# Kernel optimization log

Hardware: AMD Instinct MI355X
Metric: run time of the kernel (lower is better)

## Reference

```python
import jax, jax.numpy as jnp
import numpy as np

N, E, D, V, MAX_EDGES, G, ITERS = 50000, 200000, 128, 2000, 3, 256, 2


def _mlp3(h, W1, b1, W2, b2, W3, b3):
    h = jax.nn.relu(h @ W1 + b1)
    h = jax.nn.relu(h @ W2 + b2)
    return jax.nn.relu(h @ W3 + b3)


def _enc(ids, emb, W1, b1, W2, b2):
    h = emb[ids]
    h = jax.nn.relu(h @ W1 + b1)
    return jax.nn.relu(h @ W2 + b2)


def setup_inputs():
    key = jax.random.key(0)
    ks = iter(jax.random.split(key, 64))

    def p(shape):
        return jax.random.normal(next(ks), shape, jnp.float32) * 0.02

    inp = {
        'x': jax.random.randint(next(ks), (N,), 0, V),
        'edge_index': jax.random.randint(next(ks), (2, E), 0, N),
        'edge_attr': jax.random.randint(next(ks), (E,), 0, MAX_EDGES),
        'batch_vec': jnp.sort(jax.random.randint(next(ks), (N,), 0, G)),
        'emb_node': p((V, 2 * D)), 'Wn1': p((2 * D, D)), 'bn1': jnp.zeros((D,), jnp.float32),
        'Wn2': p((D, D)), 'bn2': jnp.zeros((D,), jnp.float32),
        'emb_edge': p((MAX_EDGES, 2 * D)), 'We1': p((2 * D, D)), 'be1': jnp.zeros((D,), jnp.float32),
        'We2': p((D, D)), 'be2': jnp.zeros((D,), jnp.float32),
    }
    for tag in ('p', 'c', 'f'):  # parent_agg, child_agg, final_agg 3-layer MLPs
        inp['W' + tag + '1'] = p((3 * D, 2 * D)); inp['b' + tag + '1'] = jnp.zeros((2 * D,), jnp.float32)
        inp['W' + tag + '2'] = p((2 * D, D)); inp['b' + tag + '2'] = jnp.zeros((D,), jnp.float32)
        inp['W' + tag + '3'] = p((D, D)); inp['b' + tag + '3'] = jnp.zeros((D,), jnp.float32)
    inp['Wo1'] = p((D, 4 * D)); inp['bo1'] = jnp.zeros((4 * D,), jnp.float32)
    inp['Wo2'] = p((4 * D, 8 * D)); inp['bo2'] = jnp.zeros((8 * D,), jnp.float32)
    return inp


def reference(x, edge_index, edge_attr, batch_vec, emb_node, Wn1, bn1, Wn2, bn2,
              emb_edge, We1, be1, We2, be2,
              Wp1, bp1, Wp2, bp2, Wp3, bp3,
              Wc1, bc1, Wc2, bc2, Wc3, bc3,
              Wf1, bf1, Wf2, bf2, Wf3, bf3,
              Wo1, bo1, Wo2, bo2):
    nodes = _enc(x, emb_node, Wn1, bn1, Wn2, bn2)       # [N, D]
    ea = _enc(edge_attr, emb_edge, We1, be1, We2, be2)  # [E, D]
    src, dst = edge_index[0], edge_index[1]
    # both aggregations normalize by degree of edge_index[0] (as in the source)
    deg = jax.ops.segment_sum(jnp.ones((E,), nodes.dtype), src, num_segments=N)
    deg_inv = jnp.where(deg > 0, 1.0 / deg, 0.0)[:, None]  # [N, 1]
    for _ in range(ITERS):
        # parent agg: flow source_to_target -> x_i = nodes[dst], x_j = nodes[src], sum at dst
        mp = _mlp3(jnp.concatenate([nodes[dst], nodes[src], ea], axis=1), Wp1, bp1, Wp2, bp2, Wp3, bp3)
        fi = deg_inv * jax.ops.segment_sum(mp, dst, num_segments=N)
        # child agg: flow target_to_source -> x_i = nodes[src], x_j = nodes[dst], sum at src
        mc = _mlp3(jnp.concatenate([nodes[src], nodes[dst], ea], axis=1), Wc1, bc1, Wc2, bc2, Wc3, bc3)
        fo = deg_inv * jax.ops.segment_sum(mc, src, num_segments=N)
        upd = _mlp3(jnp.concatenate([nodes, fi, fo], axis=1), Wf1, bf1, Wf2, bf2, Wf3, bf3)
        nodes = nodes + upd
    h = jax.nn.relu(nodes @ Wo1 + bo1)
    h = jax.nn.relu(h @ Wo2 + bo2)                      # [N, 8D]
    return jax.ops.segment_max(h, batch_vec, num_segments=G)  # global max pool [G, 8D]
```

## Files before the change

### kernel.cpp

```cpp
#include <hip/hip_runtime.h>

#define NN 50000
#define NE 200000
#define DD 128
#define GG 256
#define NITERS 2
#define NBINS 50176
#define NPART 196

typedef unsigned short u16;
typedef unsigned int u32;
typedef __bf16 bf16x8 __attribute__((ext_vector_type(8)));
typedef float f32x4 __attribute__((ext_vector_type(4)));

union U16x8 { uint4 u; bf16x8 v; u16 s[8]; };

__device__ __forceinline__ u16 f2b(float f) {
    u32 u = __float_as_uint(f);
    return (u16)((u + 0x7FFFu + ((u >> 16) & 1u)) >> 16);
}
__device__ __forceinline__ float b2f(u16 s) { return __uint_as_float(((u32)s) << 16); }

__device__ __forceinline__ uint2 pack4(const float* v) {
    uint2 r;
    r.x = (u32)f2b(v[0]) | ((u32)f2b(v[1]) << 16);
    r.y = (u32)f2b(v[2]) | ((u32)f2b(v[3]) << 16);
    return r;
}

__device__ __forceinline__ void gload_lds16(const void* g, void* lds) {
    __builtin_amdgcn_global_load_lds((const __attribute__((address_space(1))) void*)g,
                                     (__attribute__((address_space(3))) void*)lds, 16, 0, 0);
}

__device__ __forceinline__ int xcd_swz(int orig, int nwg) {
    int q = nwg >> 3, r = nwg & 7;
    int x = orig & 7, loc = orig >> 3;
    return (x < r ? x * (q + 1) : r * (q + 1) + (x - r) * q) + loc;
}

template<int K, int NL, int EPI, bool RELU, int LDN>
__global__ __launch_bounds__(256) void expand_k(
    const u16* __restrict__ A, const uint4* __restrict__ wfrag,
    const float* __restrict__ bias, float* __restrict__ of, u16* __restrict__ ob,
    int M)
{
    constexpr int KS = K / 32;
    __shared__ uint4 smem[K * 16];
    const int t = threadIdx.x, l = t & 63, wv = t >> 6;
    const int mh = wv >> 1, nh = wv & 1;
    const int mblk = blockIdx.x;

    #pragma unroll
    for (int i = 0; i < K / 16; ++i) {
        int s = t + 256 * i;
        int ln = s & 63, mt = (s >> 6) & 7, ksl = s >> 9;
        int row = mblk * 128 + mt * 16 + (ln & 15);
        if (row >= M) row = M - 1;
        int kk = ksl * 32 + (ln >> 4) * 8;
        gload_lds16(A + (size_t)row * K + kk, &smem[s - ln]);
    }
    __syncthreads();

    for (int c = 0; c < NL; ++c) {
        f32x4 acc[4][4] = {};
        #pragma unroll
        for (int ksl = 0; ksl < KS; ++ksl) {
            uint4 wa[4];
            #pragma unroll
            for (int mi = 0; mi < 4; ++mi)
                wa[mi] = wfrag[(size_t)((c * KS + ksl) * 8 + mh * 4 + mi) * 64 + l];
            bf16x8 bn[4];
            #pragma unroll
            for (int ni = 0; ni < 4; ++ni) { U16x8 u; u.u = smem[(ksl * 8 + nh * 4 + ni) * 64 + l]; bn[ni] = u.v; }
            #pragma unroll
            for (int mi = 0; mi < 4; ++mi) {
                U16x8 u; u.u = wa[mi];
                #pragma unroll
                for (int ni = 0; ni < 4; ++ni)
                    acc[mi][ni] = __builtin_amdgcn_mfma_f32_16x16x32_bf16(u.v, bn[ni], acc[mi][ni], 0, 0, 0);
            }
        }
        float4 bb[4];
        #pragma unroll
        for (int mi = 0; mi < 4; ++mi) {
            if (bias) bb[mi] = *(const float4*)(bias + c * 128 + mh * 64 + mi * 16 + 4 * (l >> 4));
            else { bb[mi].x = 0.f; bb[mi].y = 0.f; bb[mi].z = 0.f; bb[mi].w = 0.f; }
        }
        #pragma unroll
        for (int ni = 0; ni < 4; ++ni) {
            int node = mblk * 128 + nh * 64 + ni * 16 + (l & 15);
            if (node >= M) continue;
            #pragma unroll
            for (int mi = 0; mi < 4; ++mi) {
                int col = c * 128 + mh * 64 + mi * 16 + 4 * (l >> 4);
                float v[4];
                const float* bf = &bb[mi].x;
                #pragma unroll
                for (int r = 0; r < 4; ++r) {
                    v[r] = acc[mi][ni][r] + bf[r];
                    if (RELU) v[r] = fmaxf(v[r], 0.f);
                }
                if (EPI == 0) {
                    *(uint2*)(ob + (size_t)node * LDN + col) = pack4(v);
                } else {
                    size_t a = (size_t)node * 128 + col;
                    if (EPI == 2) {
                        float4 old = *(const float4*)(of + a);
                        v[0] += old.x; v[1] += old.y; v[2] += old.z; v[3] += old.w;
                    }
                    float4 s4; s4.x = v[0]; s4.y = v[1]; s4.z = v[2]; s4.w = v[3];
                    *(float4*)(of + a) = s4;
                    *(uint2*)(ob + a) = pack4(v);
                }
            }
        }
    }
}

struct SrcBf16 {
    static constexpr bool DIRECT = true;
    const u16* A; int K;
    __device__ const void* gaddr(int row, int kk) const { return A + (size_t)row * K + kk; }
    __device__ bf16x8 operator()(int row, int kk) const {
        U16x8 u; u.u = *(const uint4*)(A + (size_t)row * K + kk); return u.v;
    }
};
struct SrcEnc {
    static constexpr bool DIRECT = false;
    const float* emb; const int* xids;
    __device__ const void* gaddr(int, int) const { return nullptr; }
    __device__ bf16x8 operator()(int row, int kk) const {
        int n = xids[row];
        const float* p = emb + (size_t)n * 256 + kk;
        float4 f0 = *(const float4*)p, f1 = *(const float4*)(p + 4);
        U16x8 r;
        r.s[0]=f2b(f0.x); r.s[1]=f2b(f0.y); r.s[2]=f2b(f0.z); r.s[3]=f2b(f0.w);
        r.s[4]=f2b(f1.x); r.s[5]=f2b(f1.y); r.s[6]=f2b(f1.z); r.s[7]=f2b(f1.w);
        return r.v;
    }
};
struct SrcUpd {
    static constexpr bool DIRECT = false;
    const float* nodes; const float* fi; const float* fo; const float* deg;
    __device__ const void* gaddr(int, int) const { return nullptr; }
    __device__ bf16x8 operator()(int row, int kk) const {
        const float* s; float sc = 1.f;
        if (kk < 128) s = nodes + (size_t)row * 128 + kk;
        else {
            float d = deg[row];
            sc = d > 0.f ? 1.f / d : 0.f;
            s = (kk < 256) ? fi + (size_t)row * 128 + (kk - 128)
                           : fo + (size_t)row * 128 + (kk - 256);
        }
        float4 f0 = *(const float4*)s, f1 = *(const float4*)(s + 4);
        U16x8 r;
        r.s[0]=f2b(f0.x*sc); r.s[1]=f2b(f0.y*sc); r.s[2]=f2b(f0.z*sc); r.s[3]=f2b(f0.w*sc);
        r.s[4]=f2b(f1.x*sc); r.s[5]=f2b(f1.y*sc); r.s[6]=f2b(f1.z*sc); r.s[7]=f2b(f1.w*sc);
        return r.v;
    }
};

struct EpiArgs { float* of; u16* ob; const int* idx; int ldN; };

template<int KDIM, int NBLK, int EPI, bool RELU, class SRC>
__global__ __launch_bounds__(256) void gemm_k(SRC src, const uint4* __restrict__ wfrag,
                                              const float* __restrict__ bias,
                                              EpiArgs ea, int M)
{
    constexpr int KS = KDIM / 32;
    constexpr int NPANEL = KDIM / 64;
    __shared__ uint4 smem[2048];
    const int t = threadIdx.x;
    const int l = t & 63;
    const int wv = t >> 6;
    const int mh = wv >> 1, nh = wv & 1;
    const int ell = xcd_swz(blockIdx.x, gridDim.x);
    const int mblk = ell / NBLK, nblk = ell % NBLK;

    f32x4 acc[4][4] = {};

    for (int p = 0; p < NPANEL; ++p) {
        __syncthreads();
        if constexpr (SRC::DIRECT) {
            #pragma unroll
            for (int i = 0; i < 4; ++i) {
                int s = t + 256 * i;
                int ln = s & 63, mt = (s >> 6) & 7, ksl = s >> 9;
                int row = mblk * 128 + mt * 16 + (ln & 15);
                if (row >= M) row = M - 1;
                int kk = p * 64 + ksl * 32 + (ln >> 4) * 8;
                gload_lds16(src.gaddr(row, kk), &smem[s - ln]);
            }
        } else {
            #pragma unroll
            for (int i = 0; i < 4; ++i) {
                int s = t + 256 * i;
                int ln = s & 63, mt = (s >> 6) & 7, ksl = s >> 9;
                int row = mblk * 128 + mt * 16 + (ln & 15);
                if (row >= M) row = M - 1;
                int kk = p * 64 + ksl * 32 + (ln >> 4) * 8;
                U16x8 u; u.v = src(row, kk);
                smem[s] = u.u;
            }
        }
        {
            const uint4* wp = wfrag + (size_t)(nblk * KS + 2 * p) * 512;
            #pragma unroll
            for (int i = 0; i < 4; ++i) {
                int s = t + 256 * i;
                gload_lds16(wp + s, &smem[1024 + (s - (s & 63))]);
            }
        }
        __syncthreads();
        #pragma unroll
        for (int ksl = 0; ksl < 2; ++ksl) {
            bf16x8 a[4], b[4];
            #pragma unroll
            for (int mi = 0; mi < 4; ++mi) { U16x8 u; u.u = smem[(ksl*8 + mh*4 + mi)*64 + l]; a[mi] = u.v; }
            #pragma unroll
            for (int ni = 0; ni < 4; ++ni) { U16x8 u; u.u = smem[1024 + (ksl*8 + nh*4 + ni)*64 + l]; b[ni] = u.v; }
            #pragma unroll
            for (int mi = 0; mi < 4; ++mi)
                #pragma unroll
                for (int ni = 0; ni < 4; ++ni)
                    acc[mi][ni] = __builtin_amdgcn_mfma_f32_16x16x32_bf16(a[mi], b[ni], acc[mi][ni], 0, 0, 0);
        }
    }

    float bcol[4];
    #pragma unroll
    for (int ni = 0; ni < 4; ++ni)
        bcol[ni] = bias ? bias[nblk * 128 + nh * 64 + ni * 16 + (l & 15)] : 0.f;

    if (EPI == 0) {
        __syncthreads();
        u16* bn = (u16*)smem;
        #pragma unroll
        for (int mi = 0; mi < 4; ++mi)
            #pragma unroll
            for (int ni = 0; ni < 4; ++ni)
                #pragma unroll
                for (int r = 0; r < 4; ++r) {
                    int rl = mh * 64 + mi * 16 + (l >> 4) * 4 + r;
                    int cl = nh * 64 + ni * 16 + (l & 15);
                    float v = acc[mi][ni][r] + bcol[ni];
                    if (RELU) v = fmaxf(v, 0.f);
                    int sx = (rl >> 2) & 7;
                    bn[rl * 128 + ((((cl >> 3) ^ sx)) << 3) + (cl & 7)] = f2b(v);
                }
        __syncthreads();
        int row = t >> 1, half = t & 1;
        int grow = mblk * 128 + row;
        if (grow < M) {
            int sx = (row >> 2) & 7;
            uint4* dst = (uint4*)(ea.ob + (size_t)grow * ea.ldN + nblk * 128 + half * 64);
            const uint4* sp = ((const uint4*)bn) + row * 16;
            #pragma unroll
            for (int i = 0; i < 8; ++i) dst[i] = sp[(half * 8 + i) ^ sx];
        }
    } else if (EPI == 3) {
        int g16[4][4];
        #pragma unroll
        for (int mi = 0; mi < 4; ++mi) {
            int rb = mblk * 128 + mh * 64 + mi * 16 + (l >> 4) * 4;
            #pragma unroll
            for (int r = 0; r < 4; ++r)
                g16[mi][r] = (rb + r < M) ? ea.idx[rb + r] : -1;
        }
        #pragma unroll
        for (int ni = 0; ni < 4; ++ni) {
            int colg = nblk * 128 + nh * 64 + ni * 16 + (l & 15);
            float mv = 0.f; int cg = -1;
            #pragma unroll
            for (int mi = 0; mi < 4; ++mi)
                #pragma unroll
                for (int r = 0; r < 4; ++r) {
                    float v = acc[mi][ni][r] + bcol[ni];
                    if (RELU) v = fmaxf(v, 0.f);
                    int g = g16[mi][r];
                    if (g != cg) {
                        if (cg >= 0) atomicMax((u32*)(ea.of + (size_t)cg * 1024 + colg), __float_as_uint(mv));
                        cg = g; mv = v;
                    } else mv = fmaxf(mv, v);
                }
            if (cg >= 0) atomicMax((u32*)(ea.of + (size_t)cg * 1024 + colg), __float_as_uint(mv));
        }
    }
}

__global__ __launch_bounds__(256) void edge_fused(
    const u16* __restrict__ P, const float* __restrict__ T,
    const uint4* __restrict__ W2f, const float* __restrict__ b2,
    const uint4* __restrict__ W3f, const float* __restrict__ b3,
    const int* __restrict__ idxA, const int* __restrict__ idxB,
    const int* __restrict__ eattr, float* __restrict__ agg)
{
    __shared__ uint4 smA[2048];
    __shared__ int   sidx[3][128];
    __shared__ float sT[768];
    const int t = threadIdx.x;
    const int l = t & 63;
    const int wv = t >> 6;
    const int mh = wv >> 1, nh = wv & 1;
    const int base = xcd_swz(blockIdx.x, gridDim.x) * 128;

    if (t < 128) {
        int e = (base + t < NE) ? base + t : NE - 1;
        sidx[0][t] = idxA[e];
        sidx[1][t] = idxB[e];
        sidx[2][t] = eattr[e];
    }
    for (int i = t; i < 768; i += 256) sT[i] = T[i];
    __syncthreads();

    const int rt0 = wv * 16 + (l & 15);
    const int rt1 = (wv + 4) * 16 + (l & 15);
    const int klo = (l >> 4) * 8;
    const u16* pA[2] = { P + (size_t)sidx[0][rt0] * 512, P + (size_t)sidx[0][rt1] * 512 };
    const u16* pB[2] = { P + (size_t)sidx[1][rt0] * 512 + 256, P + (size_t)sidx[1][rt1] * 512 + 256 };
    const float* pT[2] = { sT + sidx[2][rt0] * 256, sT + sidx[2][rt1] * 256 };

    uint4 ra[4], rb[4];
    #pragma unroll
    for (int i = 0; i < 4; ++i) {
        int kk = (i >> 1) * 32 + klo;
        ra[i] = *(const uint4*)(pA[i & 1] + kk);
        rb[i] = *(const uint4*)(pB[i & 1] + kk);
    }

    f32x4 acc[4][4] = {};
    #pragma unroll
    for (int p = 0; p < 4; ++p) {
        #pragma unroll
        for (int i = 0; i < 4; ++i) {
            int kk = (i >> 1) * 32 + klo;
            U16x8 ua, ub, r;
            ua.u = ra[i]; ub.u = rb[i];
            const float* tb = pT[i & 1] + p * 64 + kk;
            #pragma unroll
            for (int j = 0; j < 8; ++j) {
                float v = b2f(ua.s[j]) + b2f(ub.s[j]) + tb[j];
                r.s[j] = f2b(fmaxf(v, 0.f));
            }
            smA[(p & 1) * 1024 + t + 256 * i] = r.u;
            if (p < 3) {
                int kn = (p + 1) * 64 + kk;
                ra[i] = *(const uint4*)(pA[i & 1] + kn);
                rb[i] = *(const uint4*)(pB[i & 1] + kn);
            }
        }
        asm volatile("s_waitcnt lgkmcnt(0)" ::: "memory");
        __builtin_amdgcn_s_barrier();
        uint4 bw[2][4];
        #pragma unroll
        for (int ksl = 0; ksl < 2; ++ksl)
            #pragma unroll
            for (int ni = 0; ni < 4; ++ni)
                bw[ksl][ni] = W2f[(size_t)((p * 2 + ksl) * 8 + nh * 4 + ni) * 64 + l];
        #pragma unroll
        for (int ksl = 0; ksl < 2; ++ksl) {
            bf16x8 a[4];
            #pragma unroll
            for (int mi = 0; mi < 4; ++mi) { U16x8 u; u.u = smA[(p & 1) * 1024 + (ksl*8 + mh*4 + mi)*64 + l]; a[mi] = u.v; }
            #pragma unroll
            for (int mi = 0; mi < 4; ++mi)
                #pragma unroll
                for (int ni = 0; ni < 4; ++ni) {
                    U16x8 u; u.u = bw[ksl][ni];
                    acc[mi][ni] = __builtin_amdgcn_mfma_f32_16x16x32_bf16(a[mi], u.v, acc[mi][ni], 0, 0, 0);
                }
        }
    }

    float bc2[4];
    #pragma unroll
    for (int ni = 0; ni < 4; ++ni) bc2[ni] = b2[nh * 64 + ni * 16 + (l & 15)];
    __builtin_amdgcn_s_barrier();
    u16* bn = (u16*)smA;
    #pragma unroll
    for (int mi = 0; mi < 4; ++mi)
        #pragma unroll
        for (int ni = 0; ni < 4; ++ni)
            #pragma unroll
            for (int r = 0; r < 4; ++r) {
                int rl = mh * 64 + mi * 16 + (l >> 4) * 4 + r;
                int cl = nh * 64 + ni * 16 + (l & 15);
                float v = fmaxf(acc[mi][ni][r] + bc2[ni], 0.f);
                int sx = (rl >> 2) & 7;
                bn[rl * 128 + (((cl >> 3) ^ sx) << 3) + (cl & 7)] = f2b(v);
            }
    asm volatile("s_waitcnt lgkmcnt(0)" ::: "memory");
    __builtin_amdgcn_s_barrier();

    f32x4 acc2[4][4] = {};
    #pragma unroll
    for (int ks = 0; ks < 4; ++ks) {
        uint4 bw[4];
        #pragma unroll
        for (int ni = 0; ni < 4; ++ni)
            bw[ni] = W3f[(size_t)(ks * 8 + nh * 4 + ni) * 64 + l];
        bf16x8 a[4];
        #pragma unroll
        for (int mi = 0; mi < 4; ++mi) {
            int rl = (mh * 4 + mi) * 16 + (l & 15);
            int c0 = ks * 32 + (l >> 4) * 8;
            int sx = (rl >> 2) & 7;
            U16x8 u; u.u = *(const uint4*)&bn[rl * 128 + (((c0 >> 3) ^ sx) << 3)];
            a[mi] = u.v;
        }
        #pragma unroll
        for (int mi = 0; mi < 4; ++mi)
            #pragma unroll
            for (int ni = 0; ni < 4; ++ni) {
                U16x8 u; u.u = bw[ni];
                acc2[mi][ni] = __builtin_amdgcn_mfma_f32_16x16x32_bf16(a[mi], u.v, acc2[mi][ni], 0, 0, 0);
            }
    }

    float bc3[4];
    #pragma unroll
    for (int ni = 0; ni < 4; ++ni) bc3[ni] = b3[nh * 64 + ni * 16 + (l & 15)];
    #pragma unroll
    for (int mi = 0; mi < 4; ++mi) {
        int rt4 = mh * 64 + mi * 16 + (l >> 4) * 4;
        int nd[4];
        #pragma unroll
        for (int r = 0; r < 4; ++r)
            nd[r] = (base + rt4 + r < NE) ? sidx[0][rt4 + r] : -1;
        #pragma unroll
        for (int ni = 0; ni < 4; ++ni) {
            int col = nh * 64 + ni * 16 + (l & 15);
            float mv = 0.f; int cg = -1;
            #pragma unroll
            for (int r = 0; r < 4; ++r) {
                float v = fmaxf(acc2[mi][ni][r] + bc3[ni], 0.f);
                if (nd[r] != cg) {
                    if (cg >= 0) atomicAdd(agg + (size_t)cg * 128 + col, mv);
                    cg = nd[r]; mv = v;
                } else mv += v;
            }
            if (cg >= 0) atomicAdd(agg + (size_t)cg * 128 + col, mv);
        }
    }
}

__global__ void hist_kernel(const int* __restrict__ key, int* __restrict__ hist)
{
    int i = blockIdx.x * 256 + threadIdx.x;
    if (i < NE) atomicAdd(&hist[key[i]], 1);
}
__global__ void chunk_sum(const int* __restrict__ h, int* __restrict__ part)
{
    __shared__ int sh[256];
    int t = threadIdx.x, b = blockIdx.x;
    sh[t] = h[b * 256 + t];
    __syncthreads();
    for (int o = 128; o > 0; o >>= 1) { if (t < o) sh[t] += sh[t + o]; __syncthreads(); }
    if (t == 0) part[b] = sh[0];
}
__global__ void scan_part(int* part)
{
    __shared__ int sh[256];
    int t = threadIdx.x;
    sh[t] = (t < NPART) ? part[t] : 0;
    __syncthreads();
    for (int o = 1; o < 256; o <<= 1) {
        int x = (t >= o) ? sh[t - o] : 0;
        __syncthreads(); sh[t] += x; __syncthreads();
    }
    if (t < NPART) part[t] = t ? sh[t - 1] : 0;
}
__global__ void mk_cursor(const int* __restrict__ h, const int* __restrict__ part,
                          int* __restrict__ cur)
{
    __shared__ int sh[256];
    int t = threadIdx.x, b = blockIdx.x;
    int v = h[b * 256 + t];
    sh[t] = v;
    __syncthreads();
    for (int o = 1; o < 256; o <<= 1) {
        int x = (t >= o) ? sh[t - o] : 0;
        __syncthreads(); sh[t] += x; __syncthreads();
    }
    cur[b * 256 + t] = part[b] + sh[t] - v;
}
__global__ void sort_scatter(const int* __restrict__ key, const int* __restrict__ oth,
                             const int* __restrict__ at, int* __restrict__ cur,
                             int* __restrict__ oA, int* __restrict__ oB, int* __restrict__ oC)
{
    int e = blockIdx.x * 256 + threadIdx.x;
    if (e < NE) {
        int k = key[e];
        int p = atomicAdd(&cur[k], 1);
        oA[p] = k; oB[p] = oth[e]; oC[p] = at[e];
    }
}

__global__ void pack_frag(const float* __restrict__ W, int ld, int rowoff, int coloff,
                          int nbs, int nbc, int KS, uint4* __restrict__ out)
{
    int tid = blockIdx.x * 256 + threadIdx.x;
    int total = nbc * KS * 512;
    if (tid >= total) return;
    int nbrel = tid / (KS * 512);
    int rem   = tid % (KS * 512);
    int ks = rem >> 9;
    int r2 = rem & 511;
    int nt = r2 >> 6, l = r2 & 63;
    int nb = nbs + nbrel;
    int k  = ks * 32 + (l >> 4) * 8;
    int col = nb * 128 + nt * 16 + (l & 15) + coloff;
    U16x8 u;
    #pragma unroll
    for (int j = 0; j < 8; ++j) u.s[j] = f2b(W[(size_t)(rowoff + k + j) * ld + col]);
    out[((size_t)(nb * KS + ks) * 8 + nt) * 64 + l] = u.u;
}

__global__ void ea_table_kernel(const float* __restrict__ emb_edge,
                                const float* __restrict__ We1, const float* __restrict__ be1,
                                const float* __restrict__ We2, const float* __restrict__ be2,
                                float* __restrict__ ea_tab)
{
    __shared__ float h1[3][128];
    const int j = threadIdx.x;
    for (int a = 0; a < 3; ++a) {
        float s = be1[j];
        for (int k = 0; k < 256; ++k) s = fmaf(emb_edge[a * 256 + k], We1[k * 128 + j], s);
        h1[a][j] = fmaxf(s, 0.f);
    }
    __syncthreads();
    for (int a = 0; a < 3; ++a) {
        float s = be2[j];
        for (int k = 0; k < 128; ++k) s = fmaf(h1[a][k], We2[k * 128 + j], s);
        ea_tab[a * 128 + j] = fmaxf(s, 0.f);
    }
}

__global__ void tpc_kernel(const float* __restrict__ ea_tab,
                           const float* __restrict__ Wp1, const float* __restrict__ bp1,
                           const float* __restrict__ Wc1, const float* __restrict__ bc1,
                           float* __restrict__ Tp, float* __restrict__ Tc)
{
    int j = threadIdx.x;
    for (int a = 0; a < 3; ++a) {
        float sp = bp1[j], sc = bc1[j];
        for (int k = 0; k < 128; ++k) {
            float e = ea_tab[a * 128 + k];
            sp = fmaf(e, Wp1[(size_t)(256 + k) * 256 + j], sp);
            sc = fmaf(e, Wc1[(size_t)(256 + k) * 256 + j], sc);
        }
        Tp[a * 256 + j] = sp;
        Tc[a * 256 + j] = sc;
    }
}

__global__ void deg_kernel(const int* __restrict__ src, float* __restrict__ deg)
{
    int i = blockIdx.x * 256 + threadIdx.x;
    if (i < NE) atomicAdd(deg + src[i], 1.0f);
}

extern "C" void kernel_launch(void* const* d_in, const int* in_sizes, int n_in,
                              void* d_out, int out_size, void* d_ws, size_t ws_size,
                              hipStream_t stream)
{
    const int*   x          = (const int*)d_in[0];
    const int*   edge_index = (const int*)d_in[1];
    const int*   edge_attr  = (const int*)d_in[2];
    const int*   batch_vec  = (const int*)d_in[3];
    const float* emb_node   = (const float*)d_in[4];
    const float* Wn1 = (const float*)d_in[5];  const float* bn1 = (const float*)d_in[6];
    const float* Wn2 = (const float*)d_in[7];  const float* bn2 = (const float*)d_in[8];
    const float* emb_edge = (const float*)d_in[9];
    const float* We1 = (const float*)d_in[10]; const float* be1 = (const float*)d_in[11];
    const float* We2 = (const float*)d_in[12]; const float* be2 = (const float*)d_in[13];
    const float* Wp1 = (const float*)d_in[14]; const float* bp1 = (const float*)d_in[15];
    const float* Wp2 = (const float*)d_in[16]; const float* bp2 = (const float*)d_in[17];
    const float* Wp3 = (const float*)d_in[18]; const float* bp3 = (const float*)d_in[19];
    const float* Wc1 = (const float*)d_in[20]; const float* bc1 = (const float*)d_in[21];
    const float* Wc2 = (const float*)d_in[22]; const float* bc2 = (const float*)d_in[23];
    const float* Wc3 = (const float*)d_in[24]; const float* bc3 = (const float*)d_in[25];
    const float* Wf1 = (const float*)d_in[26]; const float* bf1 = (const float*)d_in[27];
    const float* Wf2 = (const float*)d_in[28]; const float* bf2 = (const float*)d_in[29];
    const float* Wf3 = (const float*)d_in[30]; const float* bf3 = (const float*)d_in[31];
    const float* Wo1 = (const float*)d_in[32]; const float* bo1 = (const float*)d_in[33];
    const float* Wo2 = (const float*)d_in[34]; const float* bo2 = (const float*)d_in[35];

    float* out = (float*)d_out;

    char* w = (char*)d_ws;
    auto alloc = [&](size_t bytes) { char* p = w; w += (bytes + 255) & ~(size_t)255; return p; };
    float* nodes   = (float*)alloc((size_t)NN * DD * 4);
    u16*   nodesbf = (u16*)  alloc((size_t)NN * DD * 2);
    float* fi      = (float*)alloc((size_t)NN * DD * 4);
    float* fo      = (float*)alloc((size_t)NN * DD * 4);
    u16*   P       = (u16*)  alloc((size_t)NN * 512 * 2);
    u16*   h2      = (u16*)  alloc((size_t)NN * 384 * 2);
    float* deg     = (float*)alloc((size_t)NN * 4);
    float* ea_tab  = (float*)alloc(3 * 128 * 4);
    float* Tp      = (float*)alloc(3 * 256 * 4);
    float* Tc      = (float*)alloc(3 * 256 * 4);
    uint4* frag    = (uint4*)alloc((size_t)126976 * 16);
    int* histD = (int*)alloc(NBINS * 4);
    int* histS = (int*)alloc(NBINS * 4);
    int* partD = (int*)alloc(256 * 4);
    int* partS = (int*)alloc(256 * 4);
    int* curD  = (int*)alloc(NBINS * 4);
    int* curS  = (int*)alloc(NBINS * 4);
    int* sAp = (int*)alloc((size_t)NE * 4);
    int* sBp = (int*)alloc((size_t)NE * 4);
    int* sCp = (int*)alloc((size_t)NE * 4);
    int* sAc = (int*)alloc((size_t)NE * 4);
    int* sBc = (int*)alloc((size_t)NE * 4);
    int* sCc = (int*)alloc((size_t)NE * 4);

    u16* He = h2;
    u16* U1 = h2;
    u16* U2 = h2 + (size_t)NN * 256;
    u16* Hout1 = P;

    uint4* Wn1f = frag;
    uint4* Wn2f = Wn1f + 4096;
    uint4* PWp  = Wn2f + 2048;
    uint4* PWc  = PWp  + 8192;
    uint4* W2p  = PWc  + 8192;
    uint4* W3p  = W2p  + 4096;
    uint4* W2c  = W3p  + 2048;
    uint4* W3c  = W2c  + 4096;
    uint4* Wf1f = W3c  + 2048;
    uint4* Wf2f = Wf1f + 12288;
    uint4* Wf3f = Wf2f + 4096;
    uint4* Wo1f = Wf3f + 2048;
    uint4* Wo2f = Wo1f + 8192;

    const int* srcI = edge_index;
    const int* dstI = edge_index + NE;

    const int MB50 = (NN + 127) / 128;
    const int MBE  = (NE + 127) / 128;

    auto pk = [&](const float* W, int ld, int rowoff, int coloff, int nbs, int nbc, int KS, uint4* o) {
        int total = nbc * KS * 512;
        pack_frag<<<(total + 255) / 256, 256, 0, stream>>>(W, ld, rowoff, coloff, nbs, nbc, KS, o);
    };

    (void)hipMemsetAsync(deg, 0, (size_t)NN * 4, stream);
    (void)hipMemsetAsync(d_out, 0, (size_t)out_size * 4, stream);
    (void)hipMemsetAsync(histD, 0, NBINS * 4, stream);
    (void)hipMemsetAsync(histS, 0, NBINS * 4, stream);

    pk(Wn1, 128, 0, 0, 0, 1, 8,  Wn1f);
    pk(Wn2, 128, 0, 0, 0, 1, 4,  Wn2f);
    pk(Wp1, 256, 0,    0, 0, 2, 4, PWp);
    pk(Wp1, 256, 128, -256, 2, 2, 4, PWp);
    pk(Wc1, 256, 0,    0, 0, 2, 4, PWc);
    pk(Wc1, 256, 128, -256, 2, 2, 4, PWc);
    pk(Wp2, 128, 0, 0, 0, 1, 8,  W2p);
    pk(Wp3, 128, 0, 0, 0, 1, 4,  W3p);
    pk(Wc2, 128, 0, 0, 0, 1, 8,  W2c);
    pk(Wc3, 128, 0, 0, 0, 1, 4,  W3c);
    pk(Wf1, 256, 0, 0, 0, 2, 12, Wf1f);
    pk(Wf2, 128, 0, 0, 0, 1, 8,  Wf2f);
    pk(Wf3, 128, 0, 0, 0, 1, 4,  Wf3f);
    pk(Wo1, 512, 0, 0, 0, 4, 4,  Wo1f);
    pk(Wo2, 1024, 0, 0, 0, 8, 16, Wo2f);

    ea_table_kernel<<<1, 128, 0, stream>>>(emb_edge, We1, be1, We2, be2, ea_tab);
    tpc_kernel<<<1, 256, 0, stream>>>(ea_tab, Wp1, bp1, Wc1, bc1, Tp, Tc);
    deg_kernel<<<(NE + 255) / 256, 256, 0, stream>>>(srcI, deg);

    hist_kernel<<<(NE + 255) / 256, 256, 0, stream>>>(dstI, histD);
    hist_kernel<<<(NE + 255) / 256, 256, 0, stream>>>(srcI, histS);
    chunk_sum<<<NPART, 256, 0, stream>>>(histD, partD);
    chunk_sum<<<NPART, 256, 0, stream>>>(histS, partS);
    scan_part<<<1, 256, 0, stream>>>(partD);
    scan_part<<<1, 256, 0, stream>>>(partS);
    mk_cursor<<<NPART, 256, 0, stream>>>(histD, partD, curD);
    mk_cursor<<<NPART, 256, 0, stream>>>(histS, partS, curS);
    sort_scatter<<<(NE + 255) / 256, 256, 0, stream>>>(dstI, srcI, edge_attr, curD, sAp, sBp, sCp);
    sort_scatter<<<(NE + 255) / 256, 256, 0, stream>>>(srcI, dstI, edge_attr, curS, sAc, sBc, sCc);

    gemm_k<256, 1, 0, true, SrcEnc><<<MB50, 256, 0, stream>>>(
        SrcEnc{emb_node, x}, Wn1f, bn1, EpiArgs{nullptr, He, nullptr, 128}, NN);
    expand_k<128, 1, 1, true, 128><<<MB50, 256, 0, stream>>>(
        He, Wn2f, bn2, nodes, nodesbf, NN);

    for (int it = 0; it < NITERS; ++it) {
        (void)hipMemsetAsync(fi, 0, (size_t)2 * NN * DD * 4, stream);

        expand_k<128, 4, 0, false, 512><<<MB50, 256, 0, stream>>>(
            nodesbf, PWp, nullptr, nullptr, P, NN);
        edge_fused<<<MBE, 256, 0, stream>>>(P, Tp, W2p, bp2, W3p, bp3,
                                            sAp, sBp, sCp, fi);

        expand_k<128, 4, 0, false, 512><<<MB50, 256, 0, stream>>>(
            nodesbf, PWc, nullptr, nullptr, P, NN);
        edge_fused<<<MBE, 256, 0, stream>>>(P, Tc, W2c, bc2, W3c, bc3,
                                            sAc, sBc, sCc, fo);

        gemm_k<384, 2, 0, true, SrcUpd><<<MB50 * 2, 256, 0, stream>>>(
            SrcUpd{nodes, fi, fo, deg}, Wf1f, bf1, EpiArgs{nullptr, U1, nullptr, 256}, NN);
        expand_k<256, 1, 0, true, 128><<<MB50, 256, 0, stream>>>(
            U1, Wf2f, bf2, nullptr, U2, NN);
        expand_k<128, 1, 2, true, 128><<<MB50, 256, 0, stream>>>(
            U2, Wf3f, bf3, nodes, nodesbf, NN);
    }

    expand_k<128, 4, 0, true, 512><<<MB50, 256, 0, stream>>>(
        nodesbf, Wo1f, bo1, nullptr, Hout1, NN);
    gemm_k<512, 8, 3, true, SrcBf16><<<MB50 * 8, 256, 0, stream>>>(
        SrcBf16{Hout1, 512}, Wo2f, bo2, EpiArgs{out, nullptr, batch_vec, 1024}, NN);
}
```

Before: 971.3 us.

## Merge setup kernels, reuse src histogram as degree, split expand_k over grid y

Collapses the fifteen weight-packing launches into one table-driven pack_all kernel and merges the edge-table kernels into one. The dst and src histogram, scan, cursor and scatter passes are batched into single launches, and the src histogram doubles as the integer degree array, removing the separate degree kernel and memset. expand_k now takes its column block from blockIdx.y instead of looping over NL, so wide expansions launch four times as many blocks. In exchange, each of those blocks reloads the same A tile into shared memory.

Measured after the change: 917.0 us. 5.6% less time.

```diff
diff --git a/kernel.cpp b/kernel.cpp
--- a/kernel.cpp
+++ b/kernel.cpp
@@ -50,6 +50,7 @@
     const int t = threadIdx.x, l = t & 63, wv = t >> 6;
     const int mh = wv >> 1, nh = wv & 1;
     const int mblk = blockIdx.x;
+    const int c = blockIdx.y;
 
     #pragma unroll
     for (int i = 0; i < K / 16; ++i) {
@@ -62,57 +63,55 @@
     }
     __syncthreads();
 
-    for (int c = 0; c < NL; ++c) {
-        f32x4 acc[4][4] = {};
-        #pragma unroll
-        for (int ksl = 0; ksl < KS; ++ksl) {
-            uint4 wa[4];
-            #pragma unroll
-            for (int mi = 0; mi < 4; ++mi)
-                wa[mi] = wfrag[(size_t)((c * KS + ksl) * 8 + mh * 4 + mi) * 64 + l];
-            bf16x8 bn[4];
-            #pragma unroll
-            for (int ni = 0; ni < 4; ++ni) { U16x8 u; u.u = smem[(ksl * 8 + nh * 4 + ni) * 64 + l]; bn[ni] = u.v; }
-            #pragma unroll
-            for (int mi = 0; mi < 4; ++mi) {
-                U16x8 u; u.u = wa[mi];
-                #pragma unroll
-                for (int ni = 0; ni < 4; ++ni)
-                    acc[mi][ni] = __builtin_amdgcn_mfma_f32_16x16x32_bf16(u.v, bn[ni], acc[mi][ni], 0, 0, 0);
-            }
-        }
-        float4 bb[4];
+    f32x4 acc[4][4] = {};
+    #pragma unroll
+    for (int ksl = 0; ksl < KS; ++ksl) {
+        uint4 wa[4];
+        #pragma unroll
+        for (int mi = 0; mi < 4; ++mi)
+            wa[mi] = wfrag[(size_t)((c * KS + ksl) * 8 + mh * 4 + mi) * 64 + l];
+        bf16x8 bn[4];
+        #pragma unroll
+        for (int ni = 0; ni < 4; ++ni) { U16x8 u; u.u = smem[(ksl * 8 + nh * 4 + ni) * 64 + l]; bn[ni] = u.v; }
         #pragma unroll
         for (int mi = 0; mi < 4; ++mi) {
-            if (bias) bb[mi] = *(const float4*)(bias + c * 128 + mh * 64 + mi * 16 + 4 * (l >> 4));
-            else { bb[mi].x = 0.f; bb[mi].y = 0.f; bb[mi].z = 0.f; bb[mi].w = 0.f; }
-        }
-        #pragma unroll
-        for (int ni = 0; ni < 4; ++ni) {
-            int node = mblk * 128 + nh * 64 + ni * 16 + (l & 15);
-            if (node >= M) continue;
-            #pragma unroll
-            for (int mi = 0; mi < 4; ++mi) {
-                int col = c * 128 + mh * 64 + mi * 16 + 4 * (l >> 4);
-                float v[4];
-                const float* bf = &bb[mi].x;
-                #pragma unroll
-                for (int r = 0; r < 4; ++r) {
-                    v[r] = acc[mi][ni][r] + bf[r];
-                    if (RELU) v[r] = fmaxf(v[r], 0.f);
+            U16x8 u; u.u = wa[mi];
+            #pragma unroll
+            for (int ni = 0; ni < 4; ++ni)
+                acc[mi][ni] = __builtin_amdgcn_mfma_f32_16x16x32_bf16(u.v, bn[ni], acc[mi][ni], 0, 0, 0);
+        }
+    }
+    float4 bb[4];
+    #pragma unroll
+    for (int mi = 0; mi < 4; ++mi) {
+        if (bias) bb[mi] = *(const float4*)(bias + c * 128 + mh * 64 + mi * 16 + 4 * (l >> 4));
+        else { bb[mi].x = 0.f; bb[mi].y = 0.f; bb[mi].z = 0.f; bb[mi].w = 0.f; }
+    }
+    #pragma unroll
+    for (int ni = 0; ni < 4; ++ni) {
+        int node = mblk * 128 + nh * 64 + ni * 16 + (l & 15);
+        if (node >= M) continue;
+        #pragma unroll
+        for (int mi = 0; mi < 4; ++mi) {
+            int col = c * 128 + mh * 64 + mi * 16 + 4 * (l >> 4);
+            float v[4];
+            const float* bf = &bb[mi].x;
+            #pragma unroll
+            for (int r = 0; r < 4; ++r) {
+                v[r] = acc[mi][ni][r] + bf[r];
+                if (RELU) v[r] = fmaxf(v[r], 0.f);
+            }
+            if (EPI == 0) {
+                *(uint2*)(ob + (size_t)node * LDN + col) = pack4(v);
+            } else {
+                size_t a = (size_t)node * 128 + col;
+                if (EPI == 2) {
+                    float4 old = *(const float4*)(of + a);
+                    v[0] += old.x; v[1] += old.y; v[2] += old.z; v[3] += old.w;
                 }
-                if (EPI == 0) {
-                    *(uint2*)(ob + (size_t)node * LDN + col) = pack4(v);
-                } else {
-                    size_t a = (size_t)node * 128 + col;
-                    if (EPI == 2) {
-                        float4 old = *(const float4*)(of + a);
-                        v[0] += old.x; v[1] += old.y; v[2] += old.z; v[3] += old.w;
-                    }
-                    float4 s4; s4.x = v[0]; s4.y = v[1]; s4.z = v[2]; s4.w = v[3];
-                    *(float4*)(of + a) = s4;
-                    *(uint2*)(ob + a) = pack4(v);
-                }
+                float4 s4; s4.x = v[0]; s4.y = v[1]; s4.z = v[2]; s4.w = v[3];
+                *(float4*)(of + a) = s4;
+                *(uint2*)(ob + a) = pack4(v);
             }
         }
     }
@@ -142,14 +141,14 @@
 };
 struct SrcUpd {
     static constexpr bool DIRECT = false;
-    const float* nodes; const float* fi; const float* fo; const float* deg;
+    const float* nodes; const float* fi; const float* fo; const int* deg;
     __device__ const void* gaddr(int, int) const { return nullptr; }
     __device__ bf16x8 operator()(int row, int kk) const {
         const float* s; float sc = 1.f;
         if (kk < 128) s = nodes + (size_t)row * 128 + kk;
         else {
-            float d = deg[row];
-            sc = d > 0.f ? 1.f / d : 0.f;
+            int d = deg[row];
+            sc = d > 0 ? 1.f / (float)d : 0.f;
             s = (kk < 256) ? fi + (size_t)row * 128 + (kk - 128)
                            : fo + (size_t)row * 128 + (kk - 256);
         }
@@ -445,10 +444,12 @@
     }
 }
 
-__global__ void hist_kernel(const int* __restrict__ key, int* __restrict__ hist)
+__global__ void hist2_kernel(const int* __restrict__ dstI, const int* __restrict__ srcI,
+                             int* __restrict__ hist)
 {
     int i = blockIdx.x * 256 + threadIdx.x;
-    if (i < NE) atomicAdd(&hist[key[i]], 1);
+    if (i < NE) atomicAdd(&hist[dstI[i]], 1);
+    else if (i < 2 * NE) atomicAdd(&hist[NBINS + srcI[i - NE]], 1);
 }
 __global__ void chunk_sum(const int* __restrict__ h, int* __restrict__ part)
 {
@@ -459,17 +460,18 @@
     for (int o = 128; o > 0; o >>= 1) { if (t < o) sh[t] += sh[t + o]; __syncthreads(); }
     if (t == 0) part[b] = sh[0];
 }
-__global__ void scan_part(int* part)
+__global__ void scan_part2(int* part)
 {
     __shared__ int sh[256];
-    int t = threadIdx.x;
-    sh[t] = (t < NPART) ? part[t] : 0;
+    int t = threadIdx.x, b = blockIdx.x;
+    int* p = part + b * NPART;
+    sh[t] = (t < NPART) ? p[t] : 0;
     __syncthreads();
     for (int o = 1; o < 256; o <<= 1) {
         int x = (t >= o) ? sh[t - o] : 0;
         __syncthreads(); sh[t] += x; __syncthreads();
     }
-    if (t < NPART) part[t] = t ? sh[t - 1] : 0;
+    if (t < NPART) p[t] = (t ? sh[t - 1] : 0) + b * NE;
 }
 __global__ void mk_cursor(const int* __restrict__ h, const int* __restrict__ part,
                           int* __restrict__ cur)
@@ -485,80 +487,94 @@
     }
     cur[b * 256 + t] = part[b] + sh[t] - v;
 }
-__global__ void sort_scatter(const int* __restrict__ key, const int* __restrict__ oth,
-                             const int* __restrict__ at, int* __restrict__ cur,
-                             int* __restrict__ oA, int* __restrict__ oB, int* __restrict__ oC)
-{
-    int e = blockIdx.x * 256 + threadIdx.x;
-    if (e < NE) {
-        int k = key[e];
+__global__ void sort_scatter2(const int* __restrict__ dstI, const int* __restrict__ srcI,
+                              const int* __restrict__ at, int* __restrict__ cur,
+                              int* __restrict__ oA, int* __restrict__ oB, int* __restrict__ oC)
+{
+    int i = blockIdx.x * 256 + threadIdx.x;
+    if (i < NE) {
+        int k = dstI[i];
         int p = atomicAdd(&cur[k], 1);
-        oA[p] = k; oB[p] = oth[e]; oC[p] = at[e];
-    }
-}
-
-__global__ void pack_frag(const float* __restrict__ W, int ld, int rowoff, int coloff,
-                          int nbs, int nbc, int KS, uint4* __restrict__ out)
+        oA[p] = k; oB[p] = srcI[i]; oC[p] = at[i];
+    } else if (i < 2 * NE) {
+        int e = i - NE;
+        int k = srcI[e];
+        int p = atomicAdd(&cur[NBINS + k], 1);
+        oA[p] = k; oB[p] = dstI[e]; oC[p] = at[e];
+    }
+}
+
+struct PackPtrs { const float* p[13]; };
+
+__global__ void pack_all(PackPtrs pp, uint4* __restrict__ frag)
 {
     int tid = blockIdx.x * 256 + threadIdx.x;
-    int total = nbc * KS * 512;
-    if (tid >= total) return;
-    int nbrel = tid / (KS * 512);
-    int rem   = tid % (KS * 512);
-    int ks = rem >> 9;
-    int r2 = rem & 511;
+    if (tid >= 126976) return;
+    constexpr int NJ = 15;
+    const int   start[NJ] = {0,4096,6144,10240,14336,18432,22528,26624,28672,32768,34816,47104,51200,53248,61440};
+    const int   fbase[NJ] = {0,4096,6144,6144,14336,14336,22528,26624,28672,32768,34816,47104,51200,53248,61440};
+    const short wsel [NJ] = {0,1,2,2,3,3,4,5,6,7,8,9,10,11,12};
+    const short ldt  [NJ] = {128,128,256,256,256,256,128,128,128,128,256,128,128,512,1024};
+    const short rot  [NJ] = {0,0,0,128,0,128,0,0,0,0,0,0,0,0,0};
+    const short cot  [NJ] = {0,0,0,-256,0,-256,0,0,0,0,0,0,0,0,0};
+    const short nbst [NJ] = {0,0,0,2,0,2,0,0,0,0,0,0,0,0,0};
+    const short kst  [NJ] = {8,4,4,4,4,4,8,4,8,4,12,8,4,4,16};
+    int j = 0;
+    for (int i = NJ - 1; i >= 1; --i) if (tid >= start[i]) { j = i; break; }
+    int rem = tid - start[j];
+    int KS = kst[j];
+    int nbrel = rem / (KS * 512);
+    int r1 = rem % (KS * 512);
+    int ks = r1 >> 9;
+    int r2 = r1 & 511;
     int nt = r2 >> 6, l = r2 & 63;
-    int nb = nbs + nbrel;
+    int nb = nbst[j] + nbrel;
     int k  = ks * 32 + (l >> 4) * 8;
-    int col = nb * 128 + nt * 16 + (l & 15) + coloff;
+    int ld = ldt[j];
+    int col = nb * 128 + nt * 16 + (l & 15) + cot[j];
+    const float* W = pp.p[wsel[j]];
     U16x8 u;
     #pragma unroll
-    for (int j = 0; j < 8; ++j) u.s[j] = f2b(W[(size_t)(rowoff + k + j) * ld + col]);
-    out[((size_t)(nb * KS + ks) * 8 + nt) * 64 + l] = u.u;
-}
-
-__global__ void ea_table_kernel(const float* __restrict__ emb_edge,
-                                const float* __restrict__ We1, const float* __restrict__ be1,
-                                const float* __restrict__ We2, const float* __restrict__ be2,
-                                float* __restrict__ ea_tab)
+    for (int jj = 0; jj < 8; ++jj) u.s[jj] = f2b(W[(size_t)(rot[j] + k + jj) * ld + col]);
+    frag[fbase[j] + ((size_t)(nb * KS + ks) * 8 + nt) * 64 + l] = u.u;
+}
+
+__global__ void enc_tab_kernel(const float* __restrict__ emb_edge,
+                               const float* __restrict__ We1, const float* __restrict__ be1,
+                               const float* __restrict__ We2, const float* __restrict__ be2,
+                               const float* __restrict__ Wp1, const float* __restrict__ bp1,
+                               const float* __restrict__ Wc1, const float* __restrict__ bc1,
+                               float* __restrict__ Tp, float* __restrict__ Tc)
 {
     __shared__ float h1[3][128];
-    const int j = threadIdx.x;
-    for (int a = 0; a < 3; ++a) {
-        float s = be1[j];
-        for (int k = 0; k < 256; ++k) s = fmaf(emb_edge[a * 256 + k], We1[k * 128 + j], s);
-        h1[a][j] = fmaxf(s, 0.f);
+    __shared__ float ea[3][128];
+    const int t = threadIdx.x;
+    if (t < 128) {
+        for (int a = 0; a < 3; ++a) {
+            float s = be1[t];
+            for (int k = 0; k < 256; ++k) s = fmaf(emb_edge[a * 256 + k], We1[k * 128 + t], s);
+            h1[a][t] = fmaxf(s, 0.f);
+        }
+    }
+    __syncthreads();
+    if (t < 128) {
+        for (int a = 0; a < 3; ++a) {
+            float s = be2[t];
+            for (int k = 0; k < 128; ++k) s = fmaf(h1[a][k], We2[k * 128 + t], s);
+            ea[a][t] = fmaxf(s, 0.f);
+        }
     }
     __syncthreads();
     for (int a = 0; a < 3; ++a) {
-        float s = be2[j];
-        for (int k = 0; k < 128; ++k) s = fmaf(h1[a][k], We2[k * 128 + j], s);
-        ea_tab[a * 128 + j] = fmaxf(s, 0.f);
-    }
-}
-
-__global__ void tpc_kernel(const float* __restrict__ ea_tab,
-                           const float* __restrict__ Wp1, const float* __restrict__ bp1,
-                           const float* __restrict__ Wc1, const float* __restrict__ bc1,
-                           float* __restrict__ Tp, float* __restrict__ Tc)
-{
-    int j = threadIdx.x;
-    for (int a = 0; a < 3; ++a) {
-        float sp = bp1[j], sc = bc1[j];
+        float sp = bp1[t], sc = bc1[t];
         for (int k = 0; k < 128; ++k) {
-            float e = ea_tab[a * 128 + k];
-            sp = fmaf(e, Wp1[(size_t)(256 + k) * 256 + j], sp);
-            sc = fmaf(e, Wc1[(size_t)(256 + k) * 256 + j], sc);
-        }
-        Tp[a * 256 + j] = sp;
-        Tc[a * 256 + j] = sc;
-    }
-}
-
-__global__ void deg_kernel(const int* __restrict__ src, float* __restrict__ deg)
-{
-    int i = blockIdx.x * 256 + threadIdx.x;
-    if (i < NE) atomicAdd(deg + src[i], 1.0f);
+            float e = ea[a][k];
+            sp = fmaf(e, Wp1[(size_t)(256 + k) * 256 + t], sp);
+            sc = fmaf(e, Wc1[(size_t)(256 + k) * 256 + t], sc);
+        }
+        Tp[a * 256 + t] = sp;
+        Tc[a * 256 + t] = sc;
+    }
 }
 
 extern "C" void kernel_launch(void* const* d_in, const int* in_sizes, int n_in,
@@ -597,28 +613,21 @@
     float* fo      = (float*)alloc((size_t)NN * DD * 4);
     u16*   P       = (u16*)  alloc((size_t)NN * 512 * 2);
     u16*   h2      = (u16*)  alloc((size_t)NN * 384 * 2);
-    float* deg     = (float*)alloc((size_t)NN * 4);
-    float* ea_tab  = (float*)alloc(3 * 128 * 4);
     float* Tp      = (float*)alloc(3 * 256 * 4);
     float* Tc      = (float*)alloc(3 * 256 * 4);
     uint4* frag    = (uint4*)alloc((size_t)126976 * 16);
-    int* histD = (int*)alloc(NBINS * 4);
-    int* histS = (int*)alloc(NBINS * 4);
-    int* partD = (int*)alloc(256 * 4);
-    int* partS = (int*)alloc(256 * 4);
-    int* curD  = (int*)alloc(NBINS * 4);
-    int* curS  = (int*)alloc(NBINS * 4);
-    int* sAp = (int*)alloc((size_t)NE * 4);
-    int* sBp = (int*)alloc((size_t)NE * 4);
-    int* sCp = (int*)alloc((size_t)NE * 4);
-    int* sAc = (int*)alloc((size_t)NE * 4);
-    int* sBc = (int*)alloc((size_t)NE * 4);
-    int* sCc = (int*)alloc((size_t)NE * 4);
+    int* hist = (int*)alloc((size_t)2 * NBINS * 4);
+    int* part = (int*)alloc((size_t)2 * NPART * 4);
+    int* cur  = (int*)alloc((size_t)2 * NBINS * 4);
+    int* sA   = (int*)alloc((size_t)2 * NE * 4);
+    int* sB   = (int*)alloc((size_t)2 * NE * 4);
+    int* sC   = (int*)alloc((size_t)2 * NE * 4);
 
     u16* He = h2;
     u16* U1 = h2;
     u16* U2 = h2 + (size_t)NN * 256;
     u16* Hout1 = P;
+    const int* degS = hist + NBINS;
 
     uint4* Wn1f = frag;
     uint4* Wn2f = Wn1f + 4096;
@@ -640,74 +649,50 @@
     const int MB50 = (NN + 127) / 128;
     const int MBE  = (NE + 127) / 128;
 
-    auto pk = [&](const float* W, int ld, int rowoff, int coloff, int nbs, int nbc, int KS, uint4* o) {
-        int total = nbc * KS * 512;
-        pack_frag<<<(total + 255) / 256, 256, 0, stream>>>(W, ld, rowoff, coloff, nbs, nbc, KS, o);
-    };
-
-    (void)hipMemsetAsync(deg, 0, (size_t)NN * 4, stream);
     (void)hipMemsetAsync(d_out, 0, (size_t)out_size * 4, stream);
-    (void)hipMemsetAsync(histD, 0, NBINS * 4, stream);
-    (void)hipMemsetAsync(histS, 0, NBINS * 4, stream);
-
-    pk(Wn1, 128, 0, 0, 0, 1, 8,  Wn1f);
-    pk(Wn2, 128, 0, 0, 0, 1, 4,  Wn2f);
-    pk(Wp1, 256, 0,    0, 0, 2, 4, PWp);
-    pk(Wp1, 256, 128, -256, 2, 2, 4, PWp);
-    pk(Wc1, 256, 0,    0, 0, 2, 4, PWc);
-    pk(Wc1, 256, 128, -256, 2, 2, 4, PWc);
-    pk(Wp2, 128, 0, 0, 0, 1, 8,  W2p);
-    pk(Wp3, 128, 0, 0, 0, 1, 4,  W3p);
-    pk(Wc2, 128, 0, 0, 0, 1, 8,  W2c);
-    pk(Wc3, 128, 0, 0, 0, 1, 4,  W3c);
-    pk(Wf1, 256, 0, 0, 0, 2, 12, Wf1f);
-    pk(Wf2, 128, 0, 0, 0, 1, 8,  Wf2f);
-    pk(Wf3, 128, 0, 0, 0, 1, 4,  Wf3f);
-    pk(Wo1, 512, 0, 0, 0, 4, 4,  Wo1f);
-    pk(Wo2, 1024, 0, 0, 0, 8, 16, Wo2f);
-
-    ea_table_kernel<<<1, 128, 0, stream>>>(emb_edge, We1, be1, We2, be2, ea_tab);
-    tpc_kernel<<<1, 256, 0, stream>>>(ea_tab, Wp1, bp1, Wc1, bc1, Tp, Tc);
-    deg_kernel<<<(NE + 255) / 256, 256, 0, stream>>>(srcI, deg);
-
-    hist_kernel<<<(NE + 255) / 256, 256, 0, stream>>>(dstI, histD);
-    hist_kernel<<<(NE + 255) / 256, 256, 0, stream>>>(srcI, histS);
-    chunk_sum<<<NPART, 256, 0, stream>>>(histD, partD);
-    chunk_sum<<<NPART, 256, 0, stream>>>(histS, partS);
-    scan_part<<<1, 256, 0, stream>>>(partD);
-    scan_part<<<1, 256, 0, stream>>>(partS);
-    mk_cursor<<<NPART, 256, 0, stream>>>(histD, partD, curD);
-    mk_cursor<<<NPART, 256, 0, stream>>>(histS, partS, curS);
-    sort_scatter<<<(NE + 255) / 256, 256, 0, stream>>>(dstI, srcI, edge_attr, curD, sAp, sBp, sCp);
-    sort_scatter<<<(NE + 255) / 256, 256, 0, stream>>>(srcI, dstI, edge_attr, curS, sAc, sBc, sCc);
+    (void)hipMemsetAsync(hist, 0, (size_t)2 * NBINS * 4, stream);
+
+    PackPtrs pp;
+    pp.p[0]=Wn1; pp.p[1]=Wn2; pp.p[2]=Wp1; pp.p[3]=Wc1; pp.p[4]=Wp2; pp.p[5]=Wp3;
+    pp.p[6]=Wc2; pp.p[7]=Wc3; pp.p[8]=Wf1; pp.p[9]=Wf2; pp.p[10]=Wf3; pp.p[11]=Wo1; pp.p[12]=Wo2;
+    pack_all<<<(126976 + 255) / 256, 256, 0, stream>>>(pp, frag);
+
+    enc_tab_kernel<<<1, 256, 0, stream>>>(emb_edge, We1, be1, We2, be2,
+                                          Wp1, bp1, Wc1, bc1, Tp, Tc);
+
+    hist2_kernel<<<(2 * NE + 255) / 256, 256, 0, stream>>>(dstI, srcI, hist);
+    chunk_sum<<<2 * NPART, 256, 0, stream>>>(hist, part);
+    scan_part2<<<2, 256, 0, stream>>>(part);
+    mk_cursor<<<2 * NPART, 256, 0, stream>>>(hist, part, cur);
+    sort_scatter2<<<(2 * NE + 255) / 256, 256, 0, stream>>>(dstI, srcI, edge_attr, cur, sA, sB, sC);
 
     gemm_k<256, 1, 0, true, SrcEnc><<<MB50, 256, 0, stream>>>(
         SrcEnc{emb_node, x}, Wn1f, bn1, EpiArgs{nullptr, He, nullptr, 128}, NN);
-    expand_k<128, 1, 1, true, 128><<<MB50, 256, 0, stream>>>(
+    expand_k<128, 1, 1, true, 128><<<dim3(MB50, 1), 256, 0, stream>>>(
         He, Wn2f, bn2, nodes, nodesbf, NN);
 
     for (int it = 0; it < NITERS; ++it) {
         (void)hipMemsetAsync(fi, 0, (size_t)2 * NN * DD * 4, stream);
 
-        expand_k<128, 4, 0, false, 512><<<MB50, 256, 0, stream>>>(
+        expand_k<128, 4, 0, false, 512><<<dim3(MB50, 4), 256, 0, stream>>>(
             nodesbf, PWp, nullptr, nullptr, P, NN);
         edge_fused<<<MBE, 256, 0, stream>>>(P, Tp, W2p, bp2, W3p, bp3,
-                                            sAp, sBp, sCp, fi);
-
-        expand_k<128, 4, 0, false, 512><<<MB50, 256, 0, stream>>>(
+                                            sA, sB, sC, fi);
+
+        expand_k<128, 4, 0, false, 512><<<dim3(MB50, 4), 256, 0, stream>>>(
             nodesbf, PWc, nullptr, nullptr, P, NN);
         edge_fused<<<MBE, 256, 0, stream>>>(P, Tc, W2c, bc2, W3c, bc3,
-                                            sAc, sBc, sCc, fo);
+                                            sA + NE, sB + NE, sC + NE, fo);
 
         gemm_k<384, 2, 0, true, SrcUpd><<<MB50 * 2, 256, 0, stream>>>(
-            SrcUpd{nodes, fi, fo, deg}, Wf1f, bf1, EpiArgs{nullptr, U1, nullptr, 256}, NN);
-        expand_k<256, 1, 0, true, 128><<<MB50, 256, 0, stream>>>(
+            SrcUpd{nodes, fi, fo, degS}, Wf1f, bf1, EpiArgs{nullptr, U1, nullptr, 256}, NN);
+        expand_k<256, 1, 0, true, 128><<<dim3(MB50, 1), 256, 0, stream>>>(
             U1, Wf2f, bf2, nullptr, U2, NN);
-        expand_k<128, 1, 2, true, 128><<<MB50, 256, 0, stream>>>(
+        expand_k<128, 1, 2, true, 128><<<dim3(MB50, 1), 256, 0, stream>>>(
             U2, Wf3f, bf3, nodes, nodesbf, NN);
     }
 
-    expand_k<128, 4, 0, true, 512><<<MB50, 256, 0, stream>>>(
+    expand_k<128, 4, 0, true, 512><<<dim3(MB50, 4), 256, 0, stream>>>(
         nodesbf, Wo1f, bo1, nullptr, Hout1, NN);
     gemm_k<512, 8, 3, true, SrcBf16><<<MB50 * 8, 256, 0, stream>>>(
         SrcBf16{Hout1, 512}, Wo2f, bo2, EpiArgs{out, nullptr, batch_vec, 1024}, NN);
```
